# Performance work log

Hardware: AMD Instinct MI355X
Metric: run time of the kernel (lower is better)

The kernel has to match this reference:

```python
import jax, jax.numpy as jnp
import numpy as np

REGION = 64  # region_size r

def setup_inputs() -> dict:
    key = jax.random.key(0)
    B, C, H, W, k, r, T = 16, 64, 256, 256, 3, REGION, 32
    k0, k1, k2, k3, k4 = jax.random.split(key, 5)
    x = jax.random.normal(k0, (B, C, H, W), dtype=jnp.float32)
    weight = jax.random.normal(k1, (C, C, k, k), dtype=jnp.float32) * 0.05  # [out,in,kh,kw]
    h_idx = jax.random.randint(k2, (T,), 0, H - r + 1, dtype=jnp.int32)
    w_idx = jax.random.randint(k3, (T,), 0, W - r + 1, dtype=jnp.int32)
    lambdas = jax.random.uniform(k4, (T,), dtype=jnp.float32)
    return {"x": x, "weight": weight, "h_idx": h_idx, "w_idx": w_idx, "lambdas": lambdas}

def reference(x, weight, h_idx, w_idx, lambdas):
    B, C, H, W = x.shape
    k = weight.shape[-1]
    r = REGION
    n_r = (H // r) * (W // r)
    out_r = r - k + 1  # conv 'VALID' output size per region

    def step(out, t):
        h, w, lam = t
        crop = jax.lax.dynamic_slice(x, (0, 0, h, w), (B, C, r, r))
        c = jax.lax.conv_general_dilated(
            crop, weight, window_strides=(1, 1), padding='VALID',
            dimension_numbers=('NCHW', 'OIHW', 'NCHW'))
        cur = jax.lax.dynamic_slice(out, (0, 0, h, w), (B, C, out_r, out_r))
        out = jax.lax.dynamic_update_slice(out, cur + lam * c, (0, 0, h, w))
        return out, None

    out, _ = jax.lax.scan(step, jnp.zeros_like(x), (h_idx, w_idx, lambdas))
    return out / n_r
```

## Files before the change

### kernel.cpp

```cpp
#include <hip/hip_runtime.h>


typedef short short8 __attribute__((ext_vector_type(8)));
typedef float floatx4 __attribute__((ext_vector_type(4)));
typedef unsigned int uint4v __attribute__((ext_vector_type(4)));

#define OUTR 62

__device__ inline unsigned f2bf_pack(float lo, float hi) {
    unsigned ul = __builtin_bit_cast(unsigned, lo);
    unsigned uh = __builtin_bit_cast(unsigned, hi);
    ul = (ul + 0x7FFFu + ((ul >> 16) & 1u)) >> 16;
    uh = (uh + 0x7FFFu + ((uh >> 16) & 1u)) >> 16;
    return ul | (uh << 16);
}

__global__ void srconv_coeff_kernel(const int* __restrict__ h_idx,
                                    const int* __restrict__ w_idx,
                                    const float* __restrict__ lam,
                                    int T, float* __restrict__ coeff) {
    int p = blockIdx.x;
    int q = threadIdx.x;
    float c = 0.f;
    for (int t = 0; t < T; ++t) {
        int dh = p - h_idx[t];
        int dw = q - w_idx[t];
        if (dh >= 0 && dh < OUTR && dw >= 0 && dw < OUTR) c += lam[t];
    }
    coeff[(p << 8) + q] = c * (1.0f / 16.0f);
}

__global__ void srconv_wtrans_kernel(const float* __restrict__ wgt,
                                     uint4v* __restrict__ afrag) {
    int id = blockIdx.x * 256 + threadIdx.x;
    int l  = id & 63;
    int fi = id >> 6;
    int m  = fi & 3;
    int cb = (fi >> 2) & 1;
    int kk = fi >> 3;
    int co  = m * 16 + (l & 15);
    int ci0 = cb * 32 + (l >> 4) * 8;
    float w[8];
#pragma unroll
    for (int j = 0; j < 8; ++j)
        w[j] = wgt[(co * 64 + ci0 + j) * 9 + kk];
    uint4v d;
    d.x = f2bf_pack(w[0], w[1]);
    d.y = f2bf_pack(w[2], w[3]);
    d.z = f2bf_pack(w[4], w[5]);
    d.w = f2bf_pack(w[6], w[7]);
    afrag[id] = d;
}

__launch_bounds__(256, 2)
__global__ void srconv_fused_kernel(const float* __restrict__ x,
                                    const float* __restrict__ coeff,
                                    const short8* __restrict__ afrag,
                                    float* __restrict__ out) {
    __shared__ __align__(16) unsigned xs[2 * 340 * 16];

    const int tid  = threadIdx.x;
    const int lane = tid & 63;
    const int wv   = tid >> 6;
    const int l15  = lane & 15;
    const int kg   = lane >> 4;

    const unsigned bid = blockIdx.x;
    const unsigned swz = (bid & 7) * 512 + (bid >> 3);
    const int b    = swz >> 8;
    const int tile = swz & 255;
    const int P0   = (tile >> 3) << 3;
    const int Q0   = (tile & 7) << 5;

    float myc = coeff[((P0 + (tid >> 5)) << 8) + Q0 + (tid & 31)];
    if (__syncthreads_count(myc != 0.f) == 0) {
        const floatx4 z = (floatx4){0.f, 0.f, 0.f, 0.f};
        for (int u = tid; u < 64 * 8 * 8; u += 256) {
            int q4 = u & 7;
            int pr = (u >> 3) & 7;
            int co = u >> 6;
            *(floatx4*)(out + (((b << 6) + co) << 16) +
                        ((P0 + pr) << 8) + Q0 + (q4 << 2)) = z;
        }
        return;
    }

    const int prb = P0 + (wv << 1);

    float cf[2][2];
#pragma unroll
    for (int p = 0; p < 2; ++p)
#pragma unroll
        for (int h = 0; h < 2; ++h)
            cf[p][h] = coeff[((prb + p) << 8) + Q0 + (h << 4) + l15];

    const float* xb = x + ((size_t)b << 22);

    floatx4 va[6][2], vb[6][2];

#pragma unroll
    for (int r = 0; r < 6; ++r) {
        int u  = r * 256 + tid;
        int uc = u < 1440 ? u : 1439;
        int cp    = uc / 90;
        int rem   = uc - cp * 90;
        int row   = rem / 9;
        int chunk = rem - row * 9;
        int gr    = min(P0 + row, 255);
        int gcb   = min(Q0 + (chunk << 2), 252);
        const float* xp = xb + (cp << 17) + (gr << 8) + gcb;
        va[r][0] = *(const floatx4*)(xp);
        va[r][1] = *(const floatx4*)(xp + 65536);
    }

    short8 areg[2][4];
#pragma unroll
    for (int m = 0; m < 4; ++m) {
        areg[0][m] = afrag[(0 + m) * 64 + lane];
        areg[1][m] = afrag[(8 + m) * 64 + lane];
    }

#pragma unroll
    for (int r = 0; r < 6; ++r) {
        int u  = r * 256 + tid;
        int uc = u < 1440 ? u : 1439;
        int cp    = uc / 90;
        int rem   = uc - cp * 90;
        int row   = rem / 9;
        int chunk = rem - row * 9;
        int gr    = min(P0 + row, 255);
        int gcb   = min(Q0 + (chunk << 2), 252);
        const float* xp = xb + ((16 + cp) << 17) + (gr << 8) + gcb;
        vb[r][0] = *(const floatx4*)(xp);
        vb[r][1] = *(const floatx4*)(xp + 65536);
    }

#pragma unroll
    for (int r = 0; r < 6; ++r) {
        int u  = r * 256 + tid;
        int uc = u < 1440 ? u : 1439;
        int cp    = uc / 90;
        int rem   = uc - cp * 90;
        int row   = rem / 9;
        int chunk = rem - row * 9;
        int c4 = chunk << 2;
#pragma unroll
        for (int j = 0; j < 4; ++j) {
            if (u < 1440 && c4 + j < 34) {
                int pix = row * 34 + c4 + j;
                int slot = cp ^ (((pix >> 1) & 3) << 2);
                xs[(pix << 4) + slot] = f2bf_pack(va[r][0][j], va[r][1][j]);
            }
        }
    }
    __syncthreads();

    floatx4 acc[4][2][2];
#pragma unroll
    for (int m = 0; m < 4; ++m)
#pragma unroll
        for (int p = 0; p < 2; ++p)
#pragma unroll
            for (int h = 0; h < 2; ++h)
                acc[m][p][h] = (floatx4){0.f, 0.f, 0.f, 0.f};

#pragma unroll
    for (int t = 0; t < 9; ++t) {
        const int kh = t / 3;
        const int kw = t - kh * 3;
        const int cur = t & 1;

        short8 bf[2][2];
#pragma unroll
        for (int p = 0; p < 2; ++p)
#pragma unroll
            for (int h = 0; h < 2; ++h) {
                int prl = (wv << 1) + p + kh;
                int cl  = (h << 4) + l15 + kw;
                int pix = prl * 34 + cl;
                int off = (pix << 4) +
                          ((kg << 2) ^ (((pix >> 1) & 3) << 2));
                bf[p][h] = *(const short8*)(&xs[off]);
            }
#pragma unroll
        for (int m = 0; m < 4; ++m)
#pragma unroll
            for (int p = 0; p < 2; ++p)
#pragma unroll
                for (int h = 0; h < 2; ++h)
                    acc[m][p][h] = __builtin_amdgcn_mfma_f32_16x16x32_bf16(
                        areg[cur][m], bf[p][h], acc[m][p][h], 0, 0, 0);

        {
            const int tn  = t + 2;
            const int cbn = tn / 9;
            const int kkn = tn - cbn * 9;
#pragma unroll
            for (int m = 0; m < 4; ++m)
                areg[cur][m] =
                    afrag[((((kkn << 1) + cbn) << 2) + m) * 64 + lane];
        }
    }

#pragma unroll
    for (int r = 0; r < 6; ++r) {
        int u  = r * 256 + tid;
        int uc = u < 1440 ? u : 1439;
        int cp    = uc / 90;
        int rem   = uc - cp * 90;
        int row   = rem / 9;
        int chunk = rem - row * 9;
        int c4 = chunk << 2;
#pragma unroll
        for (int j = 0; j < 4; ++j) {
            if (u < 1440 && c4 + j < 34) {
                int pix = row * 34 + c4 + j;
                int slot = cp ^ (((pix >> 1) & 3) << 2);
                xs[5440 + (pix << 4) + slot] =
                    f2bf_pack(vb[r][0][j], vb[r][1][j]);
            }
        }
    }
    __syncthreads();

#pragma unroll
    for (int t = 9; t < 18; ++t) {
        const int kk = t - 9;
        const int kh = kk / 3;
        const int kw = kk - kh * 3;
        const int cur = t & 1;

        short8 bf[2][2];
#pragma unroll
        for (int p = 0; p < 2; ++p)
#pragma unroll
            for (int h = 0; h < 2; ++h) {
                int prl = (wv << 1) + p + kh;
                int cl  = (h << 4) + l15 + kw;
                int pix = prl * 34 + cl;
                int off = 5440 + (pix << 4) +
                          ((kg << 2) ^ (((pix >> 1) & 3) << 2));
                bf[p][h] = *(const short8*)(&xs[off]);
            }
#pragma unroll
        for (int m = 0; m < 4; ++m)
#pragma unroll
            for (int p = 0; p < 2; ++p)
#pragma unroll
                for (int h = 0; h < 2; ++h)
                    acc[m][p][h] = __builtin_amdgcn_mfma_f32_16x16x32_bf16(
                        areg[cur][m], bf[p][h], acc[m][p][h], 0, 0, 0);

        if (t < 16) {
            const int tn  = t + 2;
            const int kkn = tn - 9;
#pragma unroll
            for (int m = 0; m < 4; ++m)
                areg[cur][m] =
                    afrag[((((kkn << 1) + 1) << 2) + m) * 64 + lane];
        }
    }
    __syncthreads();

    float* epb = reinterpret_cast<float*>(xs);
    const int co_l = lane >> 3;
    const int q4   = lane & 7;

#pragma unroll
    for (int p = 0; p < 2; ++p) {
        const int pr = prb + p;
#pragma unroll
        for (int m = 0; m < 4; ++m) {
            float* ep = epb + (((wv << 1) + (m & 1)) * 576);
#pragma unroll
            for (int h = 0; h < 2; ++h)
#pragma unroll
                for (int reg = 0; reg < 4; ++reg)
                    ep[((kg << 2) + reg) * 36 + (h << 4) + l15] =
                        acc[m][p][h][reg] * cf[p][h];
#pragma unroll
            for (int j = 0; j < 2; ++j) {
                const floatx4 v = *reinterpret_cast<const floatx4*>(
                    &ep[(co_l + (j << 3)) * 36 + (q4 << 2)]);
                const int co = (m << 4) + co_l + (j << 3);
                *(floatx4*)(out + (((b << 6) + co) << 16) +
                            (pr << 8) + Q0 + (q4 << 2)) = v;
            }
        }
    }
}

extern "C" void kernel_launch(void* const* d_in, const int* in_sizes, int n_in,
                              void* d_out, int out_size, void* d_ws, size_t ws_size,
                              hipStream_t stream) {
    const float* x     = (const float*)d_in[0];
    const float* wgt   = (const float*)d_in[1];
    const int*   h_idx = (const int*)d_in[2];
    const int*   w_idx = (const int*)d_in[3];
    const float* lam   = (const float*)d_in[4];
    float*       out   = (float*)d_out;
    float*       coeff = (float*)d_ws;
    char*        af_b  = (char*)d_ws + 65536 * sizeof(float);
    const int    T     = in_sizes[2];

    srconv_coeff_kernel<<<256, 256, 0, stream>>>(h_idx, w_idx, lam, T, coeff);
    srconv_wtrans_kernel<<<18, 256, 0, stream>>>(wgt, (uint4v*)af_b);
    srconv_fused_kernel<<<4096, 256, 0, stream>>>(
        x, coeff, (const short8*)af_b, out);
}
```

Before: 177.8 us.

## Remap staging thread order, change LDS swizzle, use lightweight barriers

Changes the thread-to-element mapping for the global input loads so the low two bits of the thread index select the channel, which alters the global access pattern. The LDS XOR swizzle now uses a different pixel hash ((pix>>1)^(pix>>2)) on both the store and load sides, aimed at reducing bank conflicts. __syncthreads is replaced by a macro that waits only on LDS counters and then issues s_barrier, so outstanding global loads are not drained at each barrier. The new load mapping spreads consecutive threads across channel planes, which could weaken global coalescing.

```diff
diff --git a/kernel.cpp b/kernel.cpp
--- a/kernel.cpp
+++ b/kernel.cpp
@@ -6,6 +6,12 @@
 typedef unsigned int uint4v __attribute__((ext_vector_type(4)));
 
 #define OUTR 62
+
+#define BAR() do {                                              \
+    asm volatile("s_waitcnt lgkmcnt(0)" ::: "memory");          \
+    __builtin_amdgcn_s_barrier();                               \
+    asm volatile("" ::: "memory");                              \
+} while (0)
 
 __device__ inline unsigned f2bf_pack(float lo, float hi) {
     unsigned ul = __builtin_bit_cast(unsigned, lo);
@@ -102,12 +108,15 @@
     for (int r = 0; r < 6; ++r) {
         int u  = r * 256 + tid;
         int uc = u < 1440 ? u : 1439;
-        int cp    = uc / 90;
-        int rem   = uc - cp * 90;
-        int row   = rem / 9;
-        int chunk = rem - row * 9;
-        int gr    = min(P0 + row, 255);
-        int gcb   = min(Q0 + (chunk << 2), 252);
+        int c2   = uc & 3;
+        int v    = uc >> 2;
+        int cpHi = v / 90;
+        int pq   = v - cpHi * 90;
+        int row  = pq / 9;
+        int chunk = pq - row * 9;
+        int cp   = (cpHi << 2) | c2;
+        int gr   = min(P0 + row, 255);
+        int gcb  = min(Q0 + (chunk << 2), 252);
         const float* xp = xb + (cp << 17) + (gr << 8) + gcb;
         va[r][0] = *(const floatx4*)(xp);
         va[r][1] = *(const floatx4*)(xp + 65536);
@@ -124,12 +133,15 @@
     for (int r = 0; r < 6; ++r) {
         int u  = r * 256 + tid;
         int uc = u < 1440 ? u : 1439;
-        int cp    = uc / 90;
-        int rem   = uc - cp * 90;
-        int row   = rem / 9;
-        int chunk = rem - row * 9;
-        int gr    = min(P0 + row, 255);
-        int gcb   = min(Q0 + (chunk << 2), 252);
+        int c2   = uc & 3;
+        int v    = uc >> 2;
+        int cpHi = v / 90;
+        int pq   = v - cpHi * 90;
+        int row  = pq / 9;
+        int chunk = pq - row * 9;
+        int cp   = (cpHi << 2) | c2;
+        int gr   = min(P0 + row, 255);
+        int gcb  = min(Q0 + (chunk << 2), 252);
         const float* xp = xb + ((16 + cp) << 17) + (gr << 8) + gcb;
         vb[r][0] = *(const floatx4*)(xp);
         vb[r][1] = *(const floatx4*)(xp + 65536);
@@ -139,21 +151,24 @@
     for (int r = 0; r < 6; ++r) {
         int u  = r * 256 + tid;
         int uc = u < 1440 ? u : 1439;
-        int cp    = uc / 90;
-        int rem   = uc - cp * 90;
-        int row   = rem / 9;
-        int chunk = rem - row * 9;
+        int c2   = uc & 3;
+        int v    = uc >> 2;
+        int cpHi = v / 90;
+        int pq   = v - cpHi * 90;
+        int row  = pq / 9;
+        int chunk = pq - row * 9;
         int c4 = chunk << 2;
 #pragma unroll
         for (int j = 0; j < 4; ++j) {
             if (u < 1440 && c4 + j < 34) {
                 int pix = row * 34 + c4 + j;
-                int slot = cp ^ (((pix >> 1) & 3) << 2);
+                int f   = ((pix >> 1) ^ (pix >> 2)) & 3;
+                int slot = c2 | (((cpHi ^ f) & 3) << 2);
                 xs[(pix << 4) + slot] = f2bf_pack(va[r][0][j], va[r][1][j]);
             }
         }
     }
-    __syncthreads();
+    BAR();
 
     floatx4 acc[4][2][2];
 #pragma unroll
@@ -178,8 +193,8 @@
                 int prl = (wv << 1) + p + kh;
                 int cl  = (h << 4) + l15 + kw;
                 int pix = prl * 34 + cl;
-                int off = (pix << 4) +
-                          ((kg << 2) ^ (((pix >> 1) & 3) << 2));
+                int f   = ((pix >> 1) ^ (pix >> 2)) & 3;
+                int off = (pix << 4) + (((kg ^ f) & 3) << 2);
                 bf[p][h] = *(const short8*)(&xs[off]);
             }
 #pragma unroll
@@ -206,22 +221,25 @@
     for (int r = 0; r < 6; ++r) {
         int u  = r * 256 + tid;
         int uc = u < 1440 ? u : 1439;
-        int cp    = uc / 90;
-        int rem   = uc - cp * 90;
-        int row   = rem / 9;
-        int chunk = rem - row * 9;
+        int c2   = uc & 3;
+        int v    = uc >> 2;
+        int cpHi = v / 90;
+        int pq   = v - cpHi * 90;
+        int row  = pq / 9;
+        int chunk = pq - row * 9;
         int c4 = chunk << 2;
 #pragma unroll
         for (int j = 0; j < 4; ++j) {
             if (u < 1440 && c4 + j < 34) {
                 int pix = row * 34 + c4 + j;
-                int slot = cp ^ (((pix >> 1) & 3) << 2);
+                int f   = ((pix >> 1) ^ (pix >> 2)) & 3;
+                int slot = c2 | (((cpHi ^ f) & 3) << 2);
                 xs[5440 + (pix << 4) + slot] =
                     f2bf_pack(vb[r][0][j], vb[r][1][j]);
             }
         }
     }
-    __syncthreads();
+    BAR();
 
 #pragma unroll
     for (int t = 9; t < 18; ++t) {
@@ -238,8 +256,8 @@
                 int prl = (wv << 1) + p + kh;
                 int cl  = (h << 4) + l15 + kw;
                 int pix = prl * 34 + cl;
-                int off = 5440 + (pix << 4) +
-                          ((kg << 2) ^ (((pix >> 1) & 3) << 2));
+                int f   = ((pix >> 1) ^ (pix >> 2)) & 3;
+                int off = 5440 + (pix << 4) + (((kg ^ f) & 3) << 2);
                 bf[p][h] = *(const short8*)(&xs[off]);
             }
 #pragma unroll
@@ -260,7 +278,7 @@
                     afrag[((((kkn << 1) + 1) << 2) + m) * 64 + lane];
         }
     }
-    __syncthreads();
+    BAR();
 
     float* epb = reinterpret_cast<float*>(xs);
     const int co_l = lane >> 3;
```

Result: no change. 180.9 us (+1.8%).

## Widen conv tile to 8x64 with 512-thread blocks and single LDS buffer

Applied to the files above, without the earlier changes.

Each block now covers an 8-row by 64-column output tile with 8 waves: four waves split the rows and two split the output channels. The wider tile cuts the halo overhead of reloading the input and lowers the number of blocks. The two LDS halves become one reused buffer with an extra barrier, so the second channel half can no longer be staged while the first is still being read. Per-wave accumulators change shape from 4x2x2 to 2x2x4, and the epilogue is reorganised to give each wave its own scratch region.

```diff
diff --git a/kernel.cpp b/kernel.cpp
--- a/kernel.cpp
+++ b/kernel.cpp
@@ -52,46 +52,48 @@
     afrag[id] = d;
 }
 
-__launch_bounds__(256, 2)
+__launch_bounds__(512, 2)
 __global__ void srconv_fused_kernel(const float* __restrict__ x,
                                     const float* __restrict__ coeff,
                                     const short8* __restrict__ afrag,
                                     float* __restrict__ out) {
-    __shared__ __align__(16) unsigned xs[2 * 340 * 16];
+    __shared__ __align__(16) unsigned xs[680 * 16];
 
     const int tid  = threadIdx.x;
     const int lane = tid & 63;
     const int wv   = tid >> 6;
+    const int wvp  = wv & 3;
+    const int wvc  = wv >> 2;
     const int l15  = lane & 15;
     const int kg   = lane >> 4;
 
     const unsigned bid = blockIdx.x;
-    const unsigned swz = (bid & 7) * 512 + (bid >> 3);
-    const int b    = swz >> 8;
-    const int tile = swz & 255;
-    const int P0   = (tile >> 3) << 3;
-    const int Q0   = (tile & 7) << 5;
-
-    float myc = coeff[((P0 + (tid >> 5)) << 8) + Q0 + (tid & 31)];
+    const unsigned swz = (bid & 7) * 256 + (bid >> 3);
+    const int b    = swz >> 7;
+    const int tile = swz & 127;
+    const int P0   = (tile >> 2) << 3;
+    const int Q0   = (tile & 3) << 6;
+
+    float myc = coeff[((P0 + (tid >> 6)) << 8) + Q0 + (tid & 63)];
     if (__syncthreads_count(myc != 0.f) == 0) {
         const floatx4 z = (floatx4){0.f, 0.f, 0.f, 0.f};
-        for (int u = tid; u < 64 * 8 * 8; u += 256) {
-            int q4 = u & 7;
-            int pr = (u >> 3) & 7;
-            int co = u >> 6;
+        for (int u = tid; u < 64 * 8 * 16; u += 512) {
+            int q4 = u & 15;
+            int pr = (u >> 4) & 7;
+            int co = u >> 7;
             *(floatx4*)(out + (((b << 6) + co) << 16) +
                         ((P0 + pr) << 8) + Q0 + (q4 << 2)) = z;
         }
         return;
     }
 
-    const int prb = P0 + (wv << 1);
-
-    float cf[2][2];
+    const int prb = P0 + (wvp << 1);
+
+    float cf[2][4];
 #pragma unroll
     for (int p = 0; p < 2; ++p)
 #pragma unroll
-        for (int h = 0; h < 2; ++h)
+        for (int h = 0; h < 4; ++h)
             cf[p][h] = coeff[((prb + p) << 8) + Q0 + (h << 4) + l15];
 
     const float* xb = x + ((size_t)b << 22);
@@ -100,12 +102,12 @@
 
 #pragma unroll
     for (int r = 0; r < 6; ++r) {
-        int u  = r * 256 + tid;
-        int uc = u < 1440 ? u : 1439;
-        int cp    = uc / 90;
-        int rem   = uc - cp * 90;
-        int row   = rem / 9;
-        int chunk = rem - row * 9;
+        int u  = r * 512 + tid;
+        int uc = u < 2720 ? u : 2719;
+        int cp    = uc / 170;
+        int rem   = uc - cp * 170;
+        int row   = rem / 17;
+        int chunk = rem - row * 17;
         int gr    = min(P0 + row, 255);
         int gcb   = min(Q0 + (chunk << 2), 252);
         const float* xp = xb + (cp << 17) + (gr << 8) + gcb;
@@ -113,21 +115,22 @@
         va[r][1] = *(const floatx4*)(xp + 65536);
     }
 
-    short8 areg[2][4];
-#pragma unroll
-    for (int m = 0; m < 4; ++m) {
-        areg[0][m] = afrag[(0 + m) * 64 + lane];
-        areg[1][m] = afrag[(8 + m) * 64 + lane];
+    const int mg = wvc << 1;
+    short8 areg[2][2];
+#pragma unroll
+    for (int m = 0; m < 2; ++m) {
+        areg[0][m] = afrag[(0 + mg + m) * 64 + lane];
+        areg[1][m] = afrag[(8 + mg + m) * 64 + lane];
     }
 
 #pragma unroll
     for (int r = 0; r < 6; ++r) {
-        int u  = r * 256 + tid;
-        int uc = u < 1440 ? u : 1439;
-        int cp    = uc / 90;
-        int rem   = uc - cp * 90;
-        int row   = rem / 9;
-        int chunk = rem - row * 9;
+        int u  = r * 512 + tid;
+        int uc = u < 2720 ? u : 2719;
+        int cp    = uc / 170;
+        int rem   = uc - cp * 170;
+        int row   = rem / 17;
+        int chunk = rem - row * 17;
         int gr    = min(P0 + row, 255);
         int gcb   = min(Q0 + (chunk << 2), 252);
         const float* xp = xb + ((16 + cp) << 17) + (gr << 8) + gcb;
@@ -137,17 +140,16 @@
 
 #pragma unroll
     for (int r = 0; r < 6; ++r) {
-        int u  = r * 256 + tid;
-        int uc = u < 1440 ? u : 1439;
-        int cp    = uc / 90;
-        int rem   = uc - cp * 90;
-        int row   = rem / 9;
-        int chunk = rem - row * 9;
-        int c4 = chunk << 2;
+        int u  = r * 512 + tid;
+        int uc = u < 2720 ? u : 2719;
+        int cp    = uc / 170;
+        int rem   = uc - cp * 170;
+        int row   = rem / 17;
+        int chunk = rem - row * 17;
 #pragma unroll
         for (int j = 0; j < 4; ++j) {
-            if (u < 1440 && c4 + j < 34) {
-                int pix = row * 34 + c4 + j;
+            if (u < 2720) {
+                int pix = row * 68 + (chunk << 2) + j;
                 int slot = cp ^ (((pix >> 1) & 3) << 2);
                 xs[(pix << 4) + slot] = f2bf_pack(va[r][0][j], va[r][1][j]);
             }
@@ -155,13 +157,13 @@
     }
     __syncthreads();
 
-    floatx4 acc[4][2][2];
-#pragma unroll
-    for (int m = 0; m < 4; ++m)
+    floatx4 acc[2][2][4];
+#pragma unroll
+    for (int m = 0; m < 2; ++m)
 #pragma unroll
         for (int p = 0; p < 2; ++p)
 #pragma unroll
-            for (int h = 0; h < 2; ++h)
+            for (int h = 0; h < 4; ++h)
                 acc[m][p][h] = (floatx4){0.f, 0.f, 0.f, 0.f};
 
 #pragma unroll
@@ -170,24 +172,24 @@
         const int kw = t - kh * 3;
         const int cur = t & 1;
 
-        short8 bf[2][2];
+        short8 bf[2][4];
 #pragma unroll
         for (int p = 0; p < 2; ++p)
 #pragma unroll
-            for (int h = 0; h < 2; ++h) {
-                int prl = (wv << 1) + p + kh;
+            for (int h = 0; h < 4; ++h) {
+                int prl = (wvp << 1) + p + kh;
                 int cl  = (h << 4) + l15 + kw;
-                int pix = prl * 34 + cl;
+                int pix = prl * 68 + cl;
                 int off = (pix << 4) +
                           ((kg << 2) ^ (((pix >> 1) & 3) << 2));
                 bf[p][h] = *(const short8*)(&xs[off]);
             }
 #pragma unroll
-        for (int m = 0; m < 4; ++m)
+        for (int m = 0; m < 2; ++m)
 #pragma unroll
             for (int p = 0; p < 2; ++p)
 #pragma unroll
-                for (int h = 0; h < 2; ++h)
+                for (int h = 0; h < 4; ++h)
                     acc[m][p][h] = __builtin_amdgcn_mfma_f32_16x16x32_bf16(
                         areg[cur][m], bf[p][h], acc[m][p][h], 0, 0, 0);
 
@@ -196,28 +198,27 @@
             const int cbn = tn / 9;
             const int kkn = tn - cbn * 9;
 #pragma unroll
-            for (int m = 0; m < 4; ++m)
+            for (int m = 0; m < 2; ++m)
                 areg[cur][m] =
-                    afrag[((((kkn << 1) + cbn) << 2) + m) * 64 + lane];
-        }
-    }
+                    afrag[((((kkn << 1) + cbn) << 2) + mg + m) * 64 + lane];
+        }
+    }
+    __syncthreads();
 
 #pragma unroll
     for (int r = 0; r < 6; ++r) {
-        int u  = r * 256 + tid;
-        int uc = u < 1440 ? u : 1439;
-        int cp    = uc / 90;
-        int rem   = uc - cp * 90;
-        int row   = rem / 9;
-        int chunk = rem - row * 9;
-        int c4 = chunk << 2;
+        int u  = r * 512 + tid;
+        int uc = u < 2720 ? u : 2719;
+        int cp    = uc / 170;
+        int rem   = uc - cp * 170;
+        int row   = rem / 17;
+        int chunk = rem - row * 17;
 #pragma unroll
         for (int j = 0; j < 4; ++j) {
-            if (u < 1440 && c4 + j < 34) {
-                int pix = row * 34 + c4 + j;
+            if (u < 2720) {
+                int pix = row * 68 + (chunk << 2) + j;
                 int slot = cp ^ (((pix >> 1) & 3) << 2);
-                xs[5440 + (pix << 4) + slot] =
-                    f2bf_pack(vb[r][0][j], vb[r][1][j]);
+                xs[(pix << 4) + slot] = f2bf_pack(vb[r][0][j], vb[r][1][j]);
             }
         }
     }
@@ -230,24 +231,24 @@
         const int kw = kk - kh * 3;
         const int cur = t & 1;
 
-        short8 bf[2][2];
+        short8 bf[2][4];
 #pragma unroll
         for (int p = 0; p < 2; ++p)
 #pragma unroll
-            for (int h = 0; h < 2; ++h) {
-                int prl = (wv << 1) + p + kh;
+            for (int h = 0; h < 4; ++h) {
+                int prl = (wvp << 1) + p + kh;
                 int cl  = (h << 4) + l15 + kw;
-                int pix = prl * 34 + cl;
-                int off = 5440 + (pix << 4) +
+                int pix = prl * 68 + cl;
+                int off = (pix << 4) +
                           ((kg << 2) ^ (((pix >> 1) & 3) << 2));
                 bf[p][h] = *(const short8*)(&xs[off]);
             }
 #pragma unroll
-        for (int m = 0; m < 4; ++m)
+        for (int m = 0; m < 2; ++m)
 #pragma unroll
             for (int p = 0; p < 2; ++p)
 #pragma unroll
-                for (int h = 0; h < 2; ++h)
+                for (int h = 0; h < 4; ++h)
                     acc[m][p][h] = __builtin_amdgcn_mfma_f32_16x16x32_bf16(
                         areg[cur][m], bf[p][h], acc[m][p][h], 0, 0, 0);
 
@@ -255,34 +256,33 @@
             const int tn  = t + 2;
             const int kkn = tn - 9;
 #pragma unroll
-            for (int m = 0; m < 4; ++m)
+            for (int m = 0; m < 2; ++m)
                 areg[cur][m] =
-                    afrag[((((kkn << 1) + 1) << 2) + m) * 64 + lane];
+                    afrag[((((kkn << 1) + 1) << 2) + mg + m) * 64 + lane];
         }
     }
     __syncthreads();
 
-    float* epb = reinterpret_cast<float*>(xs);
-    const int co_l = lane >> 3;
-    const int q4   = lane & 7;
+    float* epb = reinterpret_cast<float*>(xs) + wv * 1088;
+    const int co_l = lane >> 4;
+    const int q4   = lane & 15;
 
 #pragma unroll
     for (int p = 0; p < 2; ++p) {
         const int pr = prb + p;
 #pragma unroll
-        for (int m = 0; m < 4; ++m) {
-            float* ep = epb + (((wv << 1) + (m & 1)) * 576);
-#pragma unroll
-            for (int h = 0; h < 2; ++h)
+        for (int m = 0; m < 2; ++m) {
+#pragma unroll
+            for (int h = 0; h < 4; ++h)
 #pragma unroll
                 for (int reg = 0; reg < 4; ++reg)
-                    ep[((kg << 2) + reg) * 36 + (h << 4) + l15] =
+                    epb[((kg << 2) + reg) * 68 + (h << 4) + l15] =
                         acc[m][p][h][reg] * cf[p][h];
 #pragma unroll
-            for (int j = 0; j < 2; ++j) {
+            for (int j = 0; j < 4; ++j) {
                 const floatx4 v = *reinterpret_cast<const floatx4*>(
-                    &ep[(co_l + (j << 3)) * 36 + (q4 << 2)]);
-                const int co = (m << 4) + co_l + (j << 3);
+                    &epb[(co_l + (j << 2)) * 68 + (q4 << 2)]);
+                const int co = (wvc << 5) + (m << 4) + co_l + (j << 2);
                 *(floatx4*)(out + (((b << 6) + co) << 16) +
                             (pr << 8) + Q0 + (q4 << 2)) = v;
             }
@@ -305,6 +305,6 @@
 
     srconv_coeff_kernel<<<256, 256, 0, stream>>>(h_idx, w_idx, lam, T, coeff);
     srconv_wtrans_kernel<<<18, 256, 0, stream>>>(wgt, (uint4v*)af_b);
-    srconv_fused_kernel<<<4096, 256, 0, stream>>>(
+    srconv_fused_kernel<<<2048, 512, 0, stream>>>(
         x, coeff, (const short8*)af_b, out);
 }
```

Measured after the change: 209.5 us. 1.18x slower.

## Make fused conv blocks persistent over four row strips with prefetched input halves

Applied to the files above, without the earlier changes.

Each block now handles a 32-row group as four 8-row strips instead of one strip, so the grid shrinks by four. The next strip's input is loaded from global memory while the current strip's second channel half is computed, and weight fragments stay in registers across strips. A separate LDS buffer for the epilogue, plus raw barriers, lets the staging buffer be rewritten during output stores. This aims to hide global load latency and cut per-block setup, but uses more LDS and registers and skips zero-coefficient work only at the coarser 32-row granularity.

```diff
diff --git a/kernel.cpp b/kernel.cpp
--- a/kernel.cpp
+++ b/kernel.cpp
@@ -6,6 +6,12 @@
 typedef unsigned int uint4v __attribute__((ext_vector_type(4)));
 
 #define OUTR 62
+
+#define BAR() do {                                              \
+    asm volatile("s_waitcnt lgkmcnt(0)" ::: "memory");          \
+    __builtin_amdgcn_s_barrier();                               \
+    asm volatile("" ::: "memory");                              \
+} while (0)
 
 __device__ inline unsigned f2bf_pack(float lo, float hi) {
     unsigned ul = __builtin_bit_cast(unsigned, lo);
@@ -52,52 +58,9 @@
     afrag[id] = d;
 }
 
-__launch_bounds__(256, 2)
-__global__ void srconv_fused_kernel(const float* __restrict__ x,
-                                    const float* __restrict__ coeff,
-                                    const short8* __restrict__ afrag,
-                                    float* __restrict__ out) {
-    __shared__ __align__(16) unsigned xs[2 * 340 * 16];
-
-    const int tid  = threadIdx.x;
-    const int lane = tid & 63;
-    const int wv   = tid >> 6;
-    const int l15  = lane & 15;
-    const int kg   = lane >> 4;
-
-    const unsigned bid = blockIdx.x;
-    const unsigned swz = (bid & 7) * 512 + (bid >> 3);
-    const int b    = swz >> 8;
-    const int tile = swz & 255;
-    const int P0   = (tile >> 3) << 3;
-    const int Q0   = (tile & 7) << 5;
-
-    float myc = coeff[((P0 + (tid >> 5)) << 8) + Q0 + (tid & 31)];
-    if (__syncthreads_count(myc != 0.f) == 0) {
-        const floatx4 z = (floatx4){0.f, 0.f, 0.f, 0.f};
-        for (int u = tid; u < 64 * 8 * 8; u += 256) {
-            int q4 = u & 7;
-            int pr = (u >> 3) & 7;
-            int co = u >> 6;
-            *(floatx4*)(out + (((b << 6) + co) << 16) +
-                        ((P0 + pr) << 8) + Q0 + (q4 << 2)) = z;
-        }
-        return;
-    }
-
-    const int prb = P0 + (wv << 1);
-
-    float cf[2][2];
-#pragma unroll
-    for (int p = 0; p < 2; ++p)
-#pragma unroll
-        for (int h = 0; h < 2; ++h)
-            cf[p][h] = coeff[((prb + p) << 8) + Q0 + (h << 4) + l15];
-
-    const float* xb = x + ((size_t)b << 22);
-
-    floatx4 va[6][2], vb[6][2];
-
+__device__ __forceinline__ void issue_half(const float* __restrict__ xb,
+                                           int P0, int Q0, int tid, int ciBase,
+                                           floatx4 (&v)[6][2]) {
 #pragma unroll
     for (int r = 0; r < 6; ++r) {
         int u  = r * 256 + tid;
@@ -108,33 +71,14 @@
         int chunk = rem - row * 9;
         int gr    = min(P0 + row, 255);
         int gcb   = min(Q0 + (chunk << 2), 252);
-        const float* xp = xb + (cp << 17) + (gr << 8) + gcb;
-        va[r][0] = *(const floatx4*)(xp);
-        va[r][1] = *(const floatx4*)(xp + 65536);
-    }
-
-    short8 areg[2][4];
-#pragma unroll
-    for (int m = 0; m < 4; ++m) {
-        areg[0][m] = afrag[(0 + m) * 64 + lane];
-        areg[1][m] = afrag[(8 + m) * 64 + lane];
-    }
-
-#pragma unroll
-    for (int r = 0; r < 6; ++r) {
-        int u  = r * 256 + tid;
-        int uc = u < 1440 ? u : 1439;
-        int cp    = uc / 90;
-        int rem   = uc - cp * 90;
-        int row   = rem / 9;
-        int chunk = rem - row * 9;
-        int gr    = min(P0 + row, 255);
-        int gcb   = min(Q0 + (chunk << 2), 252);
-        const float* xp = xb + ((16 + cp) << 17) + (gr << 8) + gcb;
-        vb[r][0] = *(const floatx4*)(xp);
-        vb[r][1] = *(const floatx4*)(xp + 65536);
-    }
-
+        const float* xp = xb + ((ciBase + cp) << 17) + (gr << 8) + gcb;
+        v[r][0] = *(const floatx4*)(xp);
+        v[r][1] = *(const floatx4*)(xp + 65536);
+    }
+}
+
+__device__ __forceinline__ void write_half(unsigned* __restrict__ xs, int off,
+                                           int tid, floatx4 (&v)[6][2]) {
 #pragma unroll
     for (int r = 0; r < 6; ++r) {
         int u  = r * 256 + tid;
@@ -149,144 +93,197 @@
             if (u < 1440 && c4 + j < 34) {
                 int pix = row * 34 + c4 + j;
                 int slot = cp ^ (((pix >> 1) & 3) << 2);
-                xs[(pix << 4) + slot] = f2bf_pack(va[r][0][j], va[r][1][j]);
+                xs[off + (pix << 4) + slot] = f2bf_pack(v[r][0][j], v[r][1][j]);
             }
         }
     }
-    __syncthreads();
-
-    floatx4 acc[4][2][2];
-#pragma unroll
-    for (int m = 0; m < 4; ++m)
-#pragma unroll
-        for (int p = 0; p < 2; ++p)
-#pragma unroll
-            for (int h = 0; h < 2; ++h)
-                acc[m][p][h] = (floatx4){0.f, 0.f, 0.f, 0.f};
-
-#pragma unroll
-    for (int t = 0; t < 9; ++t) {
-        const int kh = t / 3;
-        const int kw = t - kh * 3;
-        const int cur = t & 1;
-
-        short8 bf[2][2];
-#pragma unroll
-        for (int p = 0; p < 2; ++p)
-#pragma unroll
-            for (int h = 0; h < 2; ++h) {
-                int prl = (wv << 1) + p + kh;
-                int cl  = (h << 4) + l15 + kw;
-                int pix = prl * 34 + cl;
-                int off = (pix << 4) +
-                          ((kg << 2) ^ (((pix >> 1) & 3) << 2));
-                bf[p][h] = *(const short8*)(&xs[off]);
-            }
-#pragma unroll
-        for (int m = 0; m < 4; ++m)
-#pragma unroll
-            for (int p = 0; p < 2; ++p)
-#pragma unroll
-                for (int h = 0; h < 2; ++h)
-                    acc[m][p][h] = __builtin_amdgcn_mfma_f32_16x16x32_bf16(
-                        areg[cur][m], bf[p][h], acc[m][p][h], 0, 0, 0);
-
-        {
-            const int tn  = t + 2;
-            const int cbn = tn / 9;
-            const int kkn = tn - cbn * 9;
-#pragma unroll
-            for (int m = 0; m < 4; ++m)
-                areg[cur][m] =
-                    afrag[((((kkn << 1) + cbn) << 2) + m) * 64 + lane];
-        }
-    }
-
-#pragma unroll
-    for (int r = 0; r < 6; ++r) {
-        int u  = r * 256 + tid;
-        int uc = u < 1440 ? u : 1439;
-        int cp    = uc / 90;
-        int rem   = uc - cp * 90;
-        int row   = rem / 9;
-        int chunk = rem - row * 9;
-        int c4 = chunk << 2;
-#pragma unroll
-        for (int j = 0; j < 4; ++j) {
-            if (u < 1440 && c4 + j < 34) {
-                int pix = row * 34 + c4 + j;
-                int slot = cp ^ (((pix >> 1) & 3) << 2);
-                xs[5440 + (pix << 4) + slot] =
-                    f2bf_pack(vb[r][0][j], vb[r][1][j]);
-            }
-        }
-    }
-    __syncthreads();
-
-#pragma unroll
-    for (int t = 9; t < 18; ++t) {
-        const int kk = t - 9;
-        const int kh = kk / 3;
-        const int kw = kk - kh * 3;
-        const int cur = t & 1;
-
-        short8 bf[2][2];
-#pragma unroll
-        for (int p = 0; p < 2; ++p)
-#pragma unroll
-            for (int h = 0; h < 2; ++h) {
-                int prl = (wv << 1) + p + kh;
-                int cl  = (h << 4) + l15 + kw;
-                int pix = prl * 34 + cl;
-                int off = 5440 + (pix << 4) +
-                          ((kg << 2) ^ (((pix >> 1) & 3) << 2));
-                bf[p][h] = *(const short8*)(&xs[off]);
-            }
-#pragma unroll
-        for (int m = 0; m < 4; ++m)
-#pragma unroll
-            for (int p = 0; p < 2; ++p)
-#pragma unroll
-                for (int h = 0; h < 2; ++h)
-                    acc[m][p][h] = __builtin_amdgcn_mfma_f32_16x16x32_bf16(
-                        areg[cur][m], bf[p][h], acc[m][p][h], 0, 0, 0);
-
-        if (t < 16) {
-            const int tn  = t + 2;
-            const int kkn = tn - 9;
-#pragma unroll
-            for (int m = 0; m < 4; ++m)
-                areg[cur][m] =
-                    afrag[((((kkn << 1) + 1) << 2) + m) * 64 + lane];
-        }
-    }
-    __syncthreads();
-
-    float* epb = reinterpret_cast<float*>(xs);
+}
+
+__launch_bounds__(256, 2)
+__global__ void srconv_fused_kernel(const float* __restrict__ x,
+                                    const float* __restrict__ coeff,
+                                    const short8* __restrict__ afrag,
+                                    float* __restrict__ out) {
+    __shared__ __align__(16) unsigned xs[2 * 340 * 16];
+    __shared__ float ep[8 * 576];
+
+    const int tid  = threadIdx.x;
+    const int lane = tid & 63;
+    const int wv   = tid >> 6;
+    const int l15  = lane & 15;
+    const int kg   = lane >> 4;
+
+    const unsigned bid = blockIdx.x;
+    const unsigned swz = (bid & 7) * 128 + (bid >> 3);
+    const int b  = swz >> 6;
+    const int g  = swz & 63;
+    const int G0 = (g >> 3) << 5;
+    const int Q0 = (g & 7) << 5;
+
+    float cm = 0.f;
+#pragma unroll
+    for (int i = 0; i < 4; ++i) {
+        int u = i * 256 + tid;
+        cm = fmaxf(cm, coeff[((G0 + (u >> 5)) << 8) + Q0 + (u & 31)]);
+    }
+    if (__syncthreads_count(cm != 0.f) == 0) {
+        const floatx4 z = (floatx4){0.f, 0.f, 0.f, 0.f};
+        for (int u = tid; u < 64 * 32 * 8; u += 256) {
+            int q4 = u & 7;
+            int pr = (u >> 3) & 31;
+            int co = u >> 8;
+            *(floatx4*)(out + (((b << 6) + co) << 16) +
+                        ((G0 + pr) << 8) + Q0 + (q4 << 2)) = z;
+        }
+        return;
+    }
+
+    const float* xb = x + ((size_t)b << 22);
     const int co_l = lane >> 3;
     const int q4   = lane & 7;
 
-#pragma unroll
-    for (int p = 0; p < 2; ++p) {
-        const int pr = prb + p;
-#pragma unroll
-        for (int m = 0; m < 4; ++m) {
-            float* ep = epb + (((wv << 1) + (m & 1)) * 576);
+    floatx4 va[6][2], vb[6][2];
+    issue_half(xb, G0, Q0, tid, 0, va);
+
+    short8 areg[2][4];
+#pragma unroll
+    for (int m = 0; m < 4; ++m) {
+        areg[0][m] = afrag[(0 + m) * 64 + lane];
+        areg[1][m] = afrag[(8 + m) * 64 + lane];
+    }
+
+    issue_half(xb, G0, Q0, tid, 16, vb);
+    write_half(xs, 0, tid, va);
+    BAR();
+
+    for (int s = 0; s < 4; ++s) {
+        const int P0  = G0 + (s << 3);
+        const int prb = P0 + (wv << 1);
+
+        float cf[2][2];
+#pragma unroll
+        for (int p = 0; p < 2; ++p)
 #pragma unroll
             for (int h = 0; h < 2; ++h)
-#pragma unroll
-                for (int reg = 0; reg < 4; ++reg)
-                    ep[((kg << 2) + reg) * 36 + (h << 4) + l15] =
-                        acc[m][p][h][reg] * cf[p][h];
-#pragma unroll
-            for (int j = 0; j < 2; ++j) {
-                const floatx4 v = *reinterpret_cast<const floatx4*>(
-                    &ep[(co_l + (j << 3)) * 36 + (q4 << 2)]);
-                const int co = (m << 4) + co_l + (j << 3);
-                *(floatx4*)(out + (((b << 6) + co) << 16) +
-                            (pr << 8) + Q0 + (q4 << 2)) = v;
+                cf[p][h] = coeff[((prb + p) << 8) + Q0 + (h << 4) + l15];
+
+        floatx4 acc[4][2][2];
+#pragma unroll
+        for (int m = 0; m < 4; ++m)
+#pragma unroll
+            for (int p = 0; p < 2; ++p)
+#pragma unroll
+                for (int h = 0; h < 2; ++h)
+                    acc[m][p][h] = (floatx4){0.f, 0.f, 0.f, 0.f};
+
+#pragma unroll
+        for (int t = 0; t < 9; ++t) {
+            const int kh = t / 3;
+            const int kw = t - kh * 3;
+            const int cur = t & 1;
+            short8 bf[2][2];
+#pragma unroll
+            for (int p = 0; p < 2; ++p)
+#pragma unroll
+                for (int h = 0; h < 2; ++h) {
+                    int prl = (wv << 1) + p + kh;
+                    int cl  = (h << 4) + l15 + kw;
+                    int pix = prl * 34 + cl;
+                    int off = (pix << 4) +
+                              ((kg << 2) ^ (((pix >> 1) & 3) << 2));
+                    bf[p][h] = *(const short8*)(&xs[off]);
+                }
+#pragma unroll
+            for (int m = 0; m < 4; ++m)
+#pragma unroll
+                for (int p = 0; p < 2; ++p)
+#pragma unroll
+                    for (int h = 0; h < 2; ++h)
+                        acc[m][p][h] = __builtin_amdgcn_mfma_f32_16x16x32_bf16(
+                            areg[cur][m], bf[p][h], acc[m][p][h], 0, 0, 0);
+            {
+                const int tn  = (t + 2) % 18;
+                const int cbn = tn / 9;
+                const int kkn = tn - cbn * 9;
+#pragma unroll
+                for (int m = 0; m < 4; ++m)
+                    areg[cur][m] =
+                        afrag[((((kkn << 1) + cbn) << 2) + m) * 64 + lane];
             }
         }
+
+        write_half(xs, 5440, tid, vb);
+        BAR();
+
+        if (s < 3) {
+            issue_half(xb, P0 + 8, Q0, tid, 0, va);
+            issue_half(xb, P0 + 8, Q0, tid, 16, vb);
+            __builtin_amdgcn_sched_barrier(0);
+        }
+
+#pragma unroll
+        for (int t = 9; t < 18; ++t) {
+            const int kk = t - 9;
+            const int kh = kk / 3;
+            const int kw = kk - kh * 3;
+            const int cur = t & 1;
+            short8 bf[2][2];
+#pragma unroll
+            for (int p = 0; p < 2; ++p)
+#pragma unroll
+                for (int h = 0; h < 2; ++h) {
+                    int prl = (wv << 1) + p + kh;
+                    int cl  = (h << 4) + l15 + kw;
+                    int pix = prl * 34 + cl;
+                    int off = 5440 + (pix << 4) +
+                              ((kg << 2) ^ (((pix >> 1) & 3) << 2));
+                    bf[p][h] = *(const short8*)(&xs[off]);
+                }
+#pragma unroll
+            for (int m = 0; m < 4; ++m)
+#pragma unroll
+                for (int p = 0; p < 2; ++p)
+#pragma unroll
+                    for (int h = 0; h < 2; ++h)
+                        acc[m][p][h] = __builtin_amdgcn_mfma_f32_16x16x32_bf16(
+                            areg[cur][m], bf[p][h], acc[m][p][h], 0, 0, 0);
+            {
+                const int tn  = (t + 2) % 18;
+                const int cbn = tn / 9;
+                const int kkn = tn - cbn * 9;
+#pragma unroll
+                for (int m = 0; m < 4; ++m)
+                    areg[cur][m] =
+                        afrag[((((kkn << 1) + cbn) << 2) + m) * 64 + lane];
+            }
+        }
+
+        if (s < 3) write_half(xs, 0, tid, va);
+
+#pragma unroll
+        for (int p = 0; p < 2; ++p) {
+            const int pr = prb + p;
+#pragma unroll
+            for (int m = 0; m < 4; ++m) {
+                float* eps = ep + (((wv << 1) + (m & 1)) * 576);
+#pragma unroll
+                for (int h = 0; h < 2; ++h)
+#pragma unroll
+                    for (int reg = 0; reg < 4; ++reg)
+                        eps[((kg << 2) + reg) * 36 + (h << 4) + l15] =
+                            acc[m][p][h][reg] * cf[p][h];
+#pragma unroll
+                for (int j = 0; j < 2; ++j) {
+                    const floatx4 v = *reinterpret_cast<const floatx4*>(
+                        &eps[(co_l + (j << 3)) * 36 + (q4 << 2)]);
+                    const int co = (m << 4) + co_l + (j << 3);
+                    *(floatx4*)(out + (((b << 6) + co) << 16) +
+                                (pr << 8) + Q0 + (q4 << 2)) = v;
+                }
+            }
+        }
+
+        if (s < 3) BAR();
     }
 }
 
@@ -305,6 +302,6 @@
 
     srconv_coeff_kernel<<<256, 256, 0, stream>>>(h_idx, w_idx, lam, T, coeff);
     srconv_wtrans_kernel<<<18, 256, 0, stream>>>(wgt, (uint4v*)af_b);
-    srconv_fused_kernel<<<4096, 256, 0, stream>>>(
+    srconv_fused_kernel<<<1024, 256, 0, stream>>>(
         x, coeff, (const short8*)af_b, out);
 }
```

After: 612.2 us. +244.4%, slower.
